# Optimization experiments

Hardware: AMD Instinct MI355X
Metric: run time of the kernel (lower is better)

## Reference

```python
import jax, jax.numpy as jnp
import numpy as np

N, E, G = 20000, 320000, 256      # nodes, edges, graphs per batch
IN, D, P = 128, 256, 16           # input_dim, out_dim, n_prot
EPS, R, TEMP = 1e-7, 0.5, 0.2


def setup_inputs() -> dict:
    key = jax.random.key(0)
    ks = jax.random.split(key, 9)
    x = jax.random.normal(ks[0], (N, IN), jnp.float32)
    edge_index = jax.random.randint(ks[1], (2, E), 0, N)
    batch = jnp.sort(jax.random.randint(ks[2], (N,), 0, G))
    def w(k, sh):
        fan_in = sh[0]
        return jax.random.normal(k, sh, jnp.float32) * (1.0 / fan_in) ** 0.5
    return {
        "x": x, "edge_index": edge_index, "batch": batch,
        "W1": w(ks[3], (IN, D)), "b1": jnp.zeros((D,), jnp.float32),
        "W2": w(ks[4], (D, D)), "b2": jnp.zeros((D,), jnp.float32),
        "Wm1": w(ks[5], (2 * D, D)), "bm1": jnp.zeros((D,), jnp.float32),
        "Wm2": w(ks[6], (D, 1)), "bm2": jnp.zeros((1,), jnp.float32),
        "prototypes": jax.random.normal(ks[7], (P, D), jnp.float32),
    }


def _cosine(a, b):
    # prototype_distances: cosine similarity with zero-norm -> eps fixup (eval path, no softmax)
    na = jnp.linalg.norm(a, axis=1)
    na = jnp.where(na == 0, na + EPS, na)
    nb = jnp.linalg.norm(b, axis=1)
    nb = jnp.where(nb == 0, nb + EPS, nb)
    return jnp.einsum('ik,jk->ij', a, b) / (na[:, None] * nb[None, :])


def _encoder(x, src, dst, batch, W1, b1, W2, b2, atten=None):
    # 2-layer GIN: h' = relu((h + sum_{j->i} atten_ji * h_j) W + b); graph emb = sum pool
    def conv(h, W, b):
        msg = h[src]                                   # [E, d]
        if atten is not None:
            msg = msg * atten                          # [E, 1] broadcast
        agg = h + jax.ops.segment_sum(msg, dst, num_segments=N)
        return jax.nn.relu(agg @ W + b)
    h = conv(x, W1, b1)
    h = conv(h, W2, b2)
    g = jax.ops.segment_sum(h, batch, num_segments=G)  # [G, D]
    return g, h


def reference(x, edge_index, batch, W1, b1, W2, b2, Wm1, bm1, Wm2, bm2, prototypes):
    src, dst = edge_index[0], edge_index[1]
    graph_embs, node_embs = _encoder(x, src, dst, batch, W1, b1, W2, b2)

    # eval path: assign each graph to nearest prototype by cosine similarity
    sim0 = _cosine(graph_embs, prototypes)             # [G, P]
    assign_prot = jnp.argmax(sim0, axis=1)             # [G]

    # sample_subgraph (eval: plain sigmoid, no gumbel noise)
    node_proto = prototypes[assign_prot[batch]]        # [N, D]
    h = jnp.concatenate([node_embs, node_proto], axis=-1)
    node_prob = jax.nn.relu(h @ Wm1 + bm1) @ Wm2 + bm2  # [N, 1]
    node_bern = jax.nn.sigmoid(node_prob)              # [N, 1]
    edge_bern = node_bern[src] * node_bern[dst]        # [E, 1]

    x2 = x * node_bern
    subgraph_embs, _ = _encoder(x2, src, dst, batch, W1, b1, W2, b2, atten=edge_bern)

    similarity = _cosine(subgraph_embs, prototypes)    # [G, P]

    # NCE loss
    a2 = jnp.argmax(similarity, axis=1)
    onehot = jax.nn.one_hot(a2, P, dtype=similarity.dtype)
    se = jnp.exp(similarity / TEMP)
    pos = (se * onehot).sum(axis=1)
    neg = (se * (1.0 - onehot)).sum(axis=1)
    NCE_loss = -jnp.log(pos / neg).mean()

    # KL regularizers
    nb = node_bern
    KL_node = (nb * jnp.log(nb / R + EPS)
               + (1 - nb) * jnp.log((1 - nb) / (1 - R + EPS) + EPS)).mean()
    eb = edge_bern
    KL_edge = (eb * jnp.log(eb / (R * R) + EPS)
               + (1 - eb) * jnp.log((1 - eb) / (1 - R * R + EPS) + EPS)).mean()
    KL_loss = KL_node + KL_edge

    data_sim = _cosine(subgraph_embs, subgraph_embs)   # [G, G]
    return (KL_loss, NCE_loss, similarity, node_bern, edge_bern,
            data_sim, subgraph_embs, node_embs)
```

## Files before the change

kernel.cpp:

```cpp
#include <hip/hip_runtime.h>
#include <cmath>
#include <cstdint>

#define DINL __device__ __forceinline__

namespace {

constexpr int Nn = 20000, Ee = 320000, Gg = 256, Dd = 256, Pp = 16;
constexpr int Npad = 20096;
constexpr float EPSf = 1e-7f, Rf = 0.5f, TEMPf = 0.2f;

typedef unsigned short u16;
typedef __attribute__((ext_vector_type(8))) short short8;
typedef __attribute__((ext_vector_type(4))) float floatx4;

DINL float waveSum(float x) {
#pragma unroll
  for (int off = 32; off > 0; off >>= 1) x += __shfl_xor(x, off, 64);
  return x;
}

DINL u16 f2bf(float f) {
  unsigned u = __float_as_uint(f);
  unsigned r = u + 0x7fffu + ((u >> 16) & 1u);
  return (u16)(r >> 16);
}
DINL float bf2f(u16 h) { return __uint_as_float(((unsigned)h) << 16); }

__global__ void k_deg(const int* __restrict__ dst, int* __restrict__ deg) {
  int e = blockIdx.x * 256 + threadIdx.x;
  if (e < Ee) atomicAdd(&deg[dst[e]], 1);
}

__global__ __launch_bounds__(1024) void k_scan(const int* __restrict__ deg,
                                               int* __restrict__ offs) {
  __shared__ int part[1024];
  int tid = threadIdx.x;
  const int chunk = (Nn + 1023) >> 10;
  int start = tid * chunk;
  int s = 0;
  for (int k = 0; k < chunk; k++) { int i = start + k; if (i < Nn) s += deg[i]; }
  part[tid] = s;
  __syncthreads();
  for (int off = 1; off < 1024; off <<= 1) {
    int v = (tid >= off) ? part[tid - off] : 0;
    __syncthreads();
    part[tid] += v;
    __syncthreads();
  }
  int run = (tid == 0) ? 0 : part[tid - 1];
  for (int k = 0; k < chunk; k++) {
    int i = start + k;
    if (i < Nn) { offs[i] = run; run += deg[i]; }
  }
  if (start < Nn && start + chunk >= Nn) offs[Nn] = run;
}

__global__ void k_fill(const int* __restrict__ src, const int* __restrict__ dst,
                       const int* __restrict__ offs, int* __restrict__ cursor,
                       int* __restrict__ csr) {
  int e = blockIdx.x * 256 + threadIdx.x;
  if (e < Ee) {
    int d = dst[e];
    int pos = atomicAdd(&cursor[d], 1);
    csr[offs[d] + pos] = src[e];
  }
}

__global__ void k_goff(const int* __restrict__ batch, int* __restrict__ goff) {
  int i = blockIdx.x * 256 + threadIdx.x;
  if (i >= Nn) return;
  int bi = batch[i];
  int bp = (i == 0) ? -1 : batch[i - 1];
  for (int g = bp + 1; g <= bi; ++g) goff[g] = i;
  if (i == Nn - 1)
    for (int g = bi + 1; g <= Gg; ++g) goff[g] = Nn;
}

template <int DIM, int EPL, bool INBF>
DINL void slice(float r[EPL], const void* __restrict__ hv, int row, int ce) {
  if constexpr (INBF) {
    const u16* p = (const u16*)hv + (size_t)row * DIM + ce;
    ushort4 u = *(const ushort4*)p;
    r[0] = bf2f(u.x); r[1] = bf2f(u.y); r[2] = bf2f(u.z); r[3] = bf2f(u.w);
  } else {
    const float* p = (const float*)hv + (size_t)row * DIM + ce;
    float2 u = *(const float2*)p;
    r[0] = u.x; r[1] = u.y;
  }
}

template <int DIM, int MODE, bool INBF, bool OSPL>
__global__ __launch_bounds__(256) void k_aggc(
    const void* __restrict__ hv, const float* __restrict__ nb,
    const int* __restrict__ offs, const int* __restrict__ csr,
    u16* __restrict__ oh, u16* __restrict__ ol) {
  constexpr int EPL = INBF ? 4 : 2;
  constexpr int COLS = EPL * 16;
  constexpr int CHUNKS = DIM / COLS;
  int c = (int)(blockIdx.x % CHUNKS);
  int grp = (int)(blockIdx.x / CHUNKS);
  int wv = threadIdx.x >> 6, lane = threadIdx.x & 63;
  int sub = lane >> 4, l = lane & 15;
  int node = grp * 16 + wv * 4 + sub;
  if (node >= Nn) return;
  int ce = c * COLS + l * EPL;
  float self[EPL], ts[EPL];
  slice<DIM, EPL, INBF>(self, hv, node, ce);
#pragma unroll
  for (int j = 0; j < EPL; j++) ts[j] = 0.f;
  int beg = offs[node], end = offs[node + 1];
  int k = beg;
  for (; k + 4 <= end; k += 4) {
    int s0 = csr[k], s1 = csr[k + 1], s2 = csr[k + 2], s3 = csr[k + 3];
    float r0[EPL], r1[EPL], r2[EPL], r3[EPL];
    slice<DIM, EPL, INBF>(r0, hv, s0, ce);
    slice<DIM, EPL, INBF>(r1, hv, s1, ce);
    slice<DIM, EPL, INBF>(r2, hv, s2, ce);
    slice<DIM, EPL, INBF>(r3, hv, s3, ce);
    if (MODE == 0) {
#pragma unroll
      for (int j = 0; j < EPL; j++) ts[j] += (r0[j] + r1[j]) + (r2[j] + r3[j]);
    } else {
      float w0 = nb[s0], w1 = nb[s1], w2 = nb[s2], w3 = nb[s3];
      if (MODE == 1) { w0 *= w0; w1 *= w1; w2 *= w2; w3 *= w3; }
#pragma unroll
      for (int j = 0; j < EPL; j++)
        ts[j] += (w0 * r0[j] + w1 * r1[j]) + (w2 * r2[j] + w3 * r3[j]);
    }
  }
  for (; k < end; k++) {
    int s = csr[k];
    float r[EPL];
    slice<DIM, EPL, INBF>(r, hv, s, ce);
    if (MODE == 0) {
#pragma unroll
      for (int j = 0; j < EPL; j++) ts[j] += r[j];
    } else {
      float wq = nb[s];
      if (MODE == 1) wq *= wq;
#pragma unroll
      for (int j = 0; j < EPL; j++) ts[j] += wq * r[j];
    }
  }
  float val[EPL];
  if (MODE == 0) {
#pragma unroll
    for (int j = 0; j < EPL; j++) val[j] = self[j] + ts[j];
  } else if (MODE == 1) {
    float wi = nb[node];
#pragma unroll
    for (int j = 0; j < EPL; j++) val[j] = wi * (self[j] + ts[j]);
  } else {
    float wi = nb[node];
#pragma unroll
    for (int j = 0; j < EPL; j++) val[j] = self[j] + wi * ts[j];
  }
  u16 hs[EPL], ls[EPL];
#pragma unroll
  for (int j = 0; j < EPL; j++) {
    hs[j] = f2bf(val[j]);
    if (OSPL) ls[j] = f2bf(val[j] - bf2f(hs[j]));
  }
  u16* po = oh + (size_t)node * DIM + ce;
  if constexpr (EPL == 2) {
    *(ushort2*)po = make_ushort2(hs[0], hs[1]);
  } else {
    *(ushort4*)po = make_ushort4(hs[0], hs[1], hs[2], hs[3]);
  }
  if constexpr (OSPL) {
    u16* pl = ol + (size_t)node * DIM + ce;
    if constexpr (EPL == 2) {
      *(ushort2*)pl = make_ushort2(ls[0], ls[1]);
    } else {
      *(ushort4*)pl = make_ushort4(ls[0], ls[1], ls[2], ls[3]);
    }
  }
}

template <int K, bool SPLIT, int MODE>
__global__ __launch_bounds__(256) void k_mm(
    const u16* __restrict__ Ah, const u16* __restrict__ Al,
    const u16* __restrict__ Bh, const u16* __restrict__ Bl,
    const float* __restrict__ bias,
    float* __restrict__ outF, u16* __restrict__ outH, u16* __restrict__ outL,
    const float* __restrict__ pc, const int* __restrict__ batch,
    const int* __restrict__ assign, const float* __restrict__ Wm2,
    float* __restrict__ prob) {
  constexpr int SK = 40;
  __shared__ u16 AsH[128 * SK];
  __shared__ u16 AsL[SPLIT ? 128 * SK : 16];
  __shared__ u16 BsH[64 * SK];
  __shared__ u16 BsL[SPLIT ? 64 * SK : 16];
  __shared__ int ap_s[128];
  int t = threadIdx.x;
  int rowBase = blockIdx.y * 128, colBase = blockIdx.x * 64;
  if (MODE == 1 && t < 128) {
    int r = rowBase + t;
    ap_s[t] = (r < Nn) ? assign[batch[r]] : 0;
  }
  int lane = t & 63, wv = t >> 6;
  int quad = lane >> 4, l16 = lane & 15;
  int wm = wv * 32;
  floatx4 acc[2][4];
#pragma unroll
  for (int mt = 0; mt < 2; mt++)
#pragma unroll
    for (int nt = 0; nt < 4; nt++) acc[mt][nt] = (floatx4){0.f, 0.f, 0.f, 0.f};

  int ar = t >> 1;
  int akh = (t & 1) * 16;
  const u16* agH = Ah + (size_t)(rowBase + ar) * K + akh;
  const u16* agL = Al + (size_t)(rowBase + ar) * K + akh;
  int bn = t >> 2;
  int bko = (t & 3) * 8;
  const u16* bgH = Bh + (size_t)(colBase + bn) * K + bko;
  const u16* bgL = Bl + (size_t)(colBase + bn) * K + bko;

  for (int k0 = 0; k0 < K; k0 += 32) {
    uint4 a0 = *(const uint4*)(agH + k0);
    uint4 a1 = *(const uint4*)(agH + k0 + 8);
    uint4 b0 = *(const uint4*)(bgH + k0);
    uint4 a0l, a1l, b0l;
    if constexpr (SPLIT) {
      a0l = *(const uint4*)(agL + k0);
      a1l = *(const uint4*)(agL + k0 + 8);
      b0l = *(const uint4*)(bgL + k0);
    }
    __syncthreads();
    *(uint4*)&AsH[ar * SK + akh] = a0;
    *(uint4*)&AsH[ar * SK + akh + 8] = a1;
    *(uint4*)&BsH[bn * SK + bko] = b0;
    if constexpr (SPLIT) {
      *(uint4*)&AsL[ar * SK + akh] = a0l;
      *(uint4*)&AsL[ar * SK + akh + 8] = a1l;
      *(uint4*)&BsL[bn * SK + bko] = b0l;
    }
    __syncthreads();
    short8 aH[2], aL[2], bH[4], bL[4];
#pragma unroll
    for (int mt = 0; mt < 2; mt++) {
      int off = (wm + mt * 16 + l16) * SK + quad * 8;
      aH[mt] = *(const short8*)&AsH[off];
      if (SPLIT) aL[mt] = *(const short8*)&AsL[off];
    }
#pragma unroll
    for (int nt = 0; nt < 4; nt++) {
      int off = (nt * 16 + l16) * SK + quad * 8;
      bH[nt] = *(const short8*)&BsH[off];
      if (SPLIT) bL[nt] = *(const short8*)&BsL[off];
    }
#pragma unroll
    for (int mt = 0; mt < 2; mt++)
#pragma unroll
      for (int nt = 0; nt < 4; nt++) {
        acc[mt][nt] = __builtin_amdgcn_mfma_f32_16x16x32_bf16(aH[mt], bH[nt], acc[mt][nt], 0, 0, 0);
        if constexpr (SPLIT) {
          acc[mt][nt] = __builtin_amdgcn_mfma_f32_16x16x32_bf16(aH[mt], bL[nt], acc[mt][nt], 0, 0, 0);
          acc[mt][nt] = __builtin_amdgcn_mfma_f32_16x16x32_bf16(aL[mt], bH[nt], acc[mt][nt], 0, 0, 0);
        }
      }
  }

  if constexpr (MODE == 0) {
#pragma unroll
    for (int mt = 0; mt < 2; mt++)
#pragma unroll
      for (int nt = 0; nt < 4; nt++) {
        int col = colBase + nt * 16 + l16;
        float bv = bias[col];
#pragma unroll
        for (int r = 0; r < 4; r++) {
          int row = rowBase + wm + mt * 16 + quad * 4 + r;
          if (row < Nn) {
            float v = fmaxf(acc[mt][nt][r] + bv, 0.f);
            size_t o = (size_t)row * 256 + col;
            if (outF) outF[o] = v;
            if (outH) {
              u16 hh = f2bf(v);
              outH[o] = hh;
              if (outL) outL[o] = f2bf(v - bf2f(hh));
            }
          }
        }
      }
  } else {
#pragma unroll
    for (int mt = 0; mt < 2; mt++) {
      float part[4] = {0.f, 0.f, 0.f, 0.f};
#pragma unroll
      for (int nt = 0; nt < 4; nt++) {
        int col = colBase + nt * 16 + l16;
        float wmv = Wm2[col];
#pragma unroll
        for (int r = 0; r < 4; r++) {
          int lr = wm + mt * 16 + quad * 4 + r;
          int ap = ap_s[lr];
          float tv = fmaxf(acc[mt][nt][r] + pc[ap * 256 + col], 0.f);
          part[r] += tv * wmv;
        }
      }
#pragma unroll
      for (int r = 0; r < 4; r++) {
#pragma unroll
        for (int off = 1; off < 16; off <<= 1) part[r] += __shfl_xor(part[r], off, 64);
        if (l16 == 0) {
          int row = rowBase + wm + mt * 16 + quad * 4 + r;
          if (row < Nn) atomicAdd(&prob[row], part[r]);
        }
      }
    }
  }
}

__global__ __launch_bounds__(64) void k_pool(const float* __restrict__ h,
                                             const int* __restrict__ goff,
                                             float* __restrict__ gout,
                                             float* __restrict__ gout2) {
  int g = blockIdx.x, q = blockIdx.y, c = q * 64 + threadIdx.x;
  int beg = goff[g], end = goff[g + 1];
  float s = 0.f;
  for (int n = beg; n < end; ++n) s += h[(size_t)n * Dd + c];
  gout[g * Dd + c] = s;
  if (gout2 != nullptr) gout2[g * Dd + c] = s;
}

__global__ __launch_bounds__(64) void k_pc(const float* __restrict__ proto,
                                           const float* __restrict__ Wm1,
                                           const float* __restrict__ bm1,
                                           float* __restrict__ pc,
                                           float* __restrict__ pnorm) {
  int p = blockIdx.x, q = blockIdx.y, t = threadIdx.x;
  int cc = q * 64 + t;
  float s = bm1[cc];
  for (int k = 0; k < Dd; k++) s += proto[p * Dd + k] * Wm1[(size_t)(Dd + k) * Dd + cc];
  pc[p * Dd + cc] = s;
  if (q == 0) {
    float4 v = ((const float4*)(proto + (size_t)p * Dd))[t];
    float nsq = waveSum(v.x * v.x + v.y * v.y + v.z * v.z + v.w * v.w);
    if (t == 0) {
      float n = sqrtf(nsq);
      pnorm[p] = (n == 0.f) ? EPSf : n;
    }
  }
}

__global__ __launch_bounds__(64) void k_assign(const float* __restrict__ ge,
                                               const float* __restrict__ proto,
                                               const float* __restrict__ pnorm,
                                               int* __restrict__ assign) {
  int g = blockIdx.x, lane = threadIdx.x;
  float4 v = *(const float4*)(ge + (size_t)g * Dd + lane * 4);
  float na = sqrtf(waveSum(v.x * v.x + v.y * v.y + v.z * v.z + v.w * v.w));
  if (na == 0.f) na = EPSf;
  float best = -1e30f;
  int bi = 0;
#pragma unroll
  for (int p = 0; p < Pp; p++) {
    float4 w = *(const float4*)(proto + (size_t)p * Dd + lane * 4);
    float d = waveSum(v.x * w.x + v.y * w.y + v.z * w.z + v.w * w.w);
    float sim = d / (na * pnorm[p]);
    if (sim > best) { best = sim; bi = p; }
  }
  if (lane == 0) assign[g] = bi;
}

__global__ __launch_bounds__(64) void k_simnce(const float* __restrict__ se,
                                               const float* __restrict__ proto,
                                               const float* __restrict__ pnorm,
                                               float* __restrict__ osim,
                                               float* __restrict__ snorm,
                                               float* __restrict__ nceAcc) {
  int g = blockIdx.x, lane = threadIdx.x;
  float4 v = *(const float4*)(se + (size_t)g * Dd + lane * 4);
  float na = sqrtf(waveSum(v.x * v.x + v.y * v.y + v.z * v.z + v.w * v.w));
  if (na == 0.f) na = EPSf;
  float sims[Pp];
#pragma unroll
  for (int p = 0; p < Pp; p++) {
    float4 w = *(const float4*)(proto + (size_t)p * Dd + lane * 4);
    float d = waveSum(v.x * w.x + v.y * w.y + v.z * w.z + v.w * w.w);
    float sim = d / (na * pnorm[p]);
    sims[p] = sim;
    if (lane == p) osim[g * Pp + p] = sim;
  }
  float best = sims[0];
  int bi = 0;
#pragma unroll
  for (int p = 1; p < Pp; p++) {
    if (sims[p] > best) { best = sims[p]; bi = p; }
  }
  float pos = 0.f, neg = 0.f;
#pragma unroll
  for (int p = 0; p < Pp; p++) {
    float e = expf(sims[p] / TEMPf);
    if (p == bi) pos = e; else neg += e;
  }
  float lg = -logf(pos / neg);
  if (lane == 0) {
    atomicAdd(nceAcc, lg);
    snorm[g] = na;
  }
}

__global__ void k_bern(const float* __restrict__ prob, const float* __restrict__ bm2,
                       float* __restrict__ ob, float* __restrict__ accs) {
  int i = blockIdx.x * 256 + threadIdx.x;
  float val = 0.f;
  if (i < Nn) {
    float z = prob[i] + bm2[0];
    float p = 1.f / (1.f + expf(-z));
    ob[i] = p;
    const float invA = 1.f / Rf, invB = 1.f / (1.f - Rf + EPSf);
    val = p * logf(p * invA + EPSf) + (1.f - p) * logf((1.f - p) * invB + EPSf);
  }
  val = waveSum(val);
  __shared__ float wsum[4];
  int lane = threadIdx.x & 63, wvv = threadIdx.x >> 6;
  if (lane == 0) wsum[wvv] = val;
  __syncthreads();
  if (threadIdx.x == 0) atomicAdd(accs, wsum[0] + wsum[1] + wsum[2] + wsum[3]);
}

__global__ void k_eb(const int* __restrict__ src, const int* __restrict__ dst,
                     const float* __restrict__ nb, float* __restrict__ oe,
                     float* __restrict__ accs) {
  int e = blockIdx.x * 256 + threadIdx.x;
  float val = 0.f;
  if (e < Ee) {
    float v = nb[src[e]] * nb[dst[e]];
    oe[e] = v;
    const float invA = 1.f / (Rf * Rf), invB = 1.f / (1.f - Rf * Rf + EPSf);
    val = v * logf(v * invA + EPSf) + (1.f - v) * logf((1.f - v) * invB + EPSf);
  }
  val = waveSum(val);
  __shared__ float wsum[4];
  int lane = threadIdx.x & 63, wvv = threadIdx.x >> 6;
  if (lane == 0) wsum[wvv] = val;
  __syncthreads();
  if (threadIdx.x == 0) atomicAdd(accs + 1, wsum[0] + wsum[1] + wsum[2] + wsum[3]);
}

__global__ void k_fin(const float* __restrict__ accs, float* __restrict__ o_kl,
                      float* __restrict__ o_nce) {
  o_kl[0] = accs[0] / (float)Nn + accs[1] / (float)Ee;
  o_nce[0] = accs[2] / (float)Gg;
}

__global__ void k_datasim(const float* __restrict__ S, const float* __restrict__ snorm,
                          float* __restrict__ out) {
  __shared__ float si[Dd];
  int i = blockIdx.x, j = threadIdx.x;
  si[j] = S[(size_t)i * Dd + j];
  __syncthreads();
  const float4* rj = (const float4*)(S + (size_t)j * Dd);
  const float4* sif = (const float4*)si;
  float d = 0.f;
#pragma unroll 4
  for (int k = 0; k < Dd / 4; k++) {
    float4 a = sif[k];
    float4 b = rj[k];
    d += a.x * b.x + a.y * b.y + a.z * b.z + a.w * b.w;
  }
  out[(size_t)i * Gg + j] = d / (snorm[i] * snorm[j]);
}

__global__ void k_splitw(const float* __restrict__ W, u16* __restrict__ th,
                         u16* __restrict__ tl, int K) {
  int idx = blockIdx.x * 256 + threadIdx.x;
  if (idx >= K * 256) return;
  int k = idx >> 8, n = idx & 255;
  float v = W[idx];
  u16 h = f2bf(v);
  th[(size_t)n * K + k] = h;
  tl[(size_t)n * K + k] = f2bf(v - bf2f(h));
}

__global__ void k_cvtbf4(const float4* __restrict__ x, ushort4* __restrict__ o, int n4) {
  int i = blockIdx.x * 256 + threadIdx.x;
  if (i < n4) {
    float4 v = x[i];
    o[i] = make_ushort4(f2bf(v.x), f2bf(v.y), f2bf(v.z), f2bf(v.w));
  }
}

}

extern "C" void kernel_launch(void* const* d_in, const int* in_sizes, int n_in,
                              void* d_out, int out_size, void* d_ws, size_t ws_size,
                              hipStream_t stream) {
  const float* x = (const float*)d_in[0];
  const int* ei = (const int*)d_in[1];
  const int* batch = (const int*)d_in[2];
  const float* W1 = (const float*)d_in[3];
  const float* b1 = (const float*)d_in[4];
  const float* W2 = (const float*)d_in[5];
  const float* b2 = (const float*)d_in[6];
  const float* Wm1 = (const float*)d_in[7];
  const float* bm1 = (const float*)d_in[8];
  const float* Wm2 = (const float*)d_in[9];
  const float* bm2 = (const float*)d_in[10];
  const float* proto = (const float*)d_in[11];
  const int* src = ei;
  const int* dst = ei + Ee;

  float* out = (float*)d_out;
  float* o_kl = out;
  float* o_nce = out + 1;
  float* o_sim = out + 2;
  float* o_nb = o_sim + Gg * Pp;
  float* o_eb = o_nb + Nn;
  float* o_ds = o_eb + Ee;
  float* o_sg = o_ds + Gg * Gg;
  float* o_ne = o_sg + Gg * Dd;

  char* w = (char*)d_ws;
  auto take = [&](size_t bytes) -> char* {
    char* p = w;
    w += (bytes + 255) & ~(size_t)255;
    return p;
  };
  const size_t halfR = (size_t)Npad * 256 * 2;
  float* bufB = (float*)take((size_t)Npad * 256 * 4);
  char* R2 = take(2 * halfR);
  u16* A1h = (u16*)R2;
  u16* A1l = (u16*)(R2 + (size_t)Npad * 128 * 2);
  u16* A2h = (u16*)R2;
  u16* A2l = (u16*)(R2 + halfR);
  u16* h1b = (u16*)R2;
  u16* a2bh = (u16*)(R2 + halfR);
  char* R3 = take(2 * halfR);
  u16* neh = (u16*)R3;
  u16* nel = (u16*)(R3 + halfR);
  u16* a1bh = (u16*)R3;
  u16* xbf = (u16*)(R3 + halfR);

  int* csr = (int*)take((size_t)Ee * 4);
  int* deg = (int*)take((size_t)Nn * 4);
  int* cursor = (int*)take((size_t)Nn * 4);
  int* offs = (int*)take((size_t)(Nn + 1) * 4);
  int* goff = (int*)take((size_t)(Gg + 1) * 4);
  float* gemb = (float*)take((size_t)Gg * Dd * 4);
  float* sgemb = (float*)take((size_t)Gg * Dd * 4);
  float* pcb = (float*)take((size_t)Pp * Dd * 4);
  float* pnorm = (float*)take(Pp * 4);
  int* assign = (int*)take(Gg * 4);
  float* snorm = (float*)take(Gg * 4);
  float* prob = (float*)take(Nn * 4);
  float* accs = (float*)take(16);
  u16* W1th = (u16*)take((size_t)256 * 128 * 2);
  u16* W1tl = (u16*)take((size_t)256 * 128 * 2);
  u16* W2th = (u16*)take((size_t)256 * 256 * 2);
  u16* W2tl = (u16*)take((size_t)256 * 256 * 2);
  u16* Wm1th = (u16*)take((size_t)256 * 256 * 2);
  u16* Wm1tl = (u16*)take((size_t)256 * 256 * 2);

  hipMemsetAsync(deg, 0, 2 * 80128, stream);
  hipMemsetAsync(prob, 0, 80128 + 16, stream);

  const int eB = (Ee + 255) / 256;
  const int nB = (Nn + 255) / 256;
  dim3 gmm(4, 157);

  k_deg<<<eB, 256, 0, stream>>>(dst, deg);
  k_scan<<<1, 1024, 0, stream>>>(deg, offs);
  k_fill<<<eB, 256, 0, stream>>>(src, dst, offs, cursor, csr);
  k_goff<<<nB, 256, 0, stream>>>(batch, goff);
  k_pc<<<dim3(Pp, 4), 64, 0, stream>>>(proto, Wm1, bm1, pcb, pnorm);
  k_splitw<<<(128 * 256 + 255) / 256, 256, 0, stream>>>(W1, W1th, W1tl, 128);
  k_splitw<<<(256 * 256 + 255) / 256, 256, 0, stream>>>(W2, W2th, W2tl, 256);
  k_splitw<<<(256 * 256 + 255) / 256, 256, 0, stream>>>(Wm1, Wm1th, Wm1tl, 256);

  k_aggc<128, 0, false, true><<<1250 * 4, 256, 0, stream>>>(x, nullptr, offs, csr, A1h, A1l);
  k_mm<128, true, 0><<<gmm, 256, 0, stream>>>(A1h, A1l, W1th, W1tl, b1, bufB, nullptr,
                                              nullptr, nullptr, nullptr, nullptr,
                                              nullptr, nullptr);
  k_aggc<256, 0, false, true><<<1250 * 8, 256, 0, stream>>>(bufB, nullptr, offs, csr, A2h, A2l);
  k_mm<256, true, 0><<<gmm, 256, 0, stream>>>(A2h, A2l, W2th, W2tl, b2, o_ne, neh, nel,
                                              nullptr, nullptr, nullptr, nullptr,
                                              nullptr);
  k_pool<<<dim3(Gg, 4), 64, 0, stream>>>(o_ne, goff, gemb, nullptr);
  k_assign<<<Gg, 64, 0, stream>>>(gemb, proto, pnorm, assign);
  k_mm<256, true, 1><<<gmm, 256, 0, stream>>>(neh, nel, Wm1th, Wm1tl, nullptr, nullptr,
                                              nullptr, nullptr, pcb, batch, assign,
                                              Wm2, prob);
  k_bern<<<nB, 256, 0, stream>>>(prob, bm2, o_nb, accs);
  k_eb<<<eB, 256, 0, stream>>>(src, dst, o_nb, o_eb, accs);

  k_cvtbf4<<<(Nn * 128 / 4 + 255) / 256, 256, 0, stream>>>((const float4*)x,
                                                           (ushort4*)xbf, Nn * 128 / 4);
  k_aggc<128, 1, true, false><<<1250 * 2, 256, 0, stream>>>(xbf, o_nb, offs, csr, a1bh, nullptr);
  k_mm<128, false, 0><<<gmm, 256, 0, stream>>>(a1bh, nullptr, W1th, nullptr, b1, nullptr,
                                               h1b, nullptr, nullptr, nullptr, nullptr,
                                               nullptr, nullptr);
  k_aggc<256, 2, true, false><<<1250 * 4, 256, 0, stream>>>(h1b, o_nb, offs, csr, a2bh, nullptr);
  k_mm<256, false, 0><<<gmm, 256, 0, stream>>>(a2bh, nullptr, W2th, nullptr, b2, bufB,
                                               nullptr, nullptr, nullptr, nullptr,
                                               nullptr, nullptr, nullptr);
  k_pool<<<dim3(Gg, 4), 64, 0, stream>>>(bufB, goff, sgemb, o_sg);

  k_simnce<<<Gg, 64, 0, stream>>>(sgemb, proto, pnorm, o_sim, snorm, accs + 2);
  k_fin<<<1, 1, 0, stream>>>(accs, o_kl, o_nce);
  k_datasim<<<Gg, 256, 0, stream>>>(sgemb, snorm, o_ds);
}
```

Measured before the change: 473.3 us.

## Fuse small kernels and add nontemporal loads/stores across aggregation and GEMM

```diff
diff --git a/kernel.cpp b/kernel.cpp
--- a/kernel.cpp
+++ b/kernel.cpp
@@ -13,6 +13,8 @@
 typedef unsigned short u16;
 typedef __attribute__((ext_vector_type(8))) short short8;
 typedef __attribute__((ext_vector_type(4))) float floatx4;
+typedef __attribute__((ext_vector_type(2))) unsigned int u2v;
+typedef __attribute__((ext_vector_type(4))) unsigned int u4v;
 
 DINL float waveSum(float x) {
 #pragma unroll
@@ -32,28 +34,40 @@
   if (e < Ee) atomicAdd(&deg[dst[e]], 1);
 }
 
-__global__ __launch_bounds__(1024) void k_scan(const int* __restrict__ deg,
-                                               int* __restrict__ offs) {
-  __shared__ int part[1024];
+__global__ __launch_bounds__(1024) void k_pre(const int* __restrict__ deg,
+                                              int* __restrict__ offs,
+                                              const int* __restrict__ batch,
+                                              int* __restrict__ goff) {
   int tid = threadIdx.x;
-  const int chunk = (Nn + 1023) >> 10;
-  int start = tid * chunk;
-  int s = 0;
-  for (int k = 0; k < chunk; k++) { int i = start + k; if (i < Nn) s += deg[i]; }
-  part[tid] = s;
-  __syncthreads();
-  for (int off = 1; off < 1024; off <<= 1) {
-    int v = (tid >= off) ? part[tid - off] : 0;
+  if (blockIdx.x == 0) {
+    __shared__ int part[1024];
+    const int chunk = (Nn + 1023) >> 10;
+    int start = tid * chunk;
+    int s = 0;
+    for (int k = 0; k < chunk; k++) { int i = start + k; if (i < Nn) s += deg[i]; }
+    part[tid] = s;
     __syncthreads();
-    part[tid] += v;
-    __syncthreads();
-  }
-  int run = (tid == 0) ? 0 : part[tid - 1];
-  for (int k = 0; k < chunk; k++) {
-    int i = start + k;
-    if (i < Nn) { offs[i] = run; run += deg[i]; }
-  }
-  if (start < Nn && start + chunk >= Nn) offs[Nn] = run;
+    for (int off = 1; off < 1024; off <<= 1) {
+      int v = (tid >= off) ? part[tid - off] : 0;
+      __syncthreads();
+      part[tid] += v;
+      __syncthreads();
+    }
+    int run = (tid == 0) ? 0 : part[tid - 1];
+    for (int k = 0; k < chunk; k++) {
+      int i = start + k;
+      if (i < Nn) { offs[i] = run; run += deg[i]; }
+    }
+    if (start < Nn && start + chunk >= Nn) offs[Nn] = run;
+  } else {
+    for (int i = tid; i < Nn; i += 1024) {
+      int bi = batch[i];
+      int bp = (i == 0) ? -1 : batch[i - 1];
+      for (int g = bp + 1; g <= bi; ++g) goff[g] = i;
+      if (i == Nn - 1)
+        for (int g = bi + 1; g <= Gg; ++g) goff[g] = Nn;
+    }
+  }
 }
 
 __global__ void k_fill(const int* __restrict__ src, const int* __restrict__ dst,
@@ -65,16 +79,6 @@
     int pos = atomicAdd(&cursor[d], 1);
     csr[offs[d] + pos] = src[e];
   }
-}
-
-__global__ void k_goff(const int* __restrict__ batch, int* __restrict__ goff) {
-  int i = blockIdx.x * 256 + threadIdx.x;
-  if (i >= Nn) return;
-  int bi = batch[i];
-  int bp = (i == 0) ? -1 : batch[i - 1];
-  for (int g = bp + 1; g <= bi; ++g) goff[g] = i;
-  if (i == Nn - 1)
-    for (int g = bi + 1; g <= Gg; ++g) goff[g] = Nn;
 }
 
 template <int DIM, int EPL, bool INBF>
@@ -164,21 +168,29 @@
   }
   u16* po = oh + (size_t)node * DIM + ce;
   if constexpr (EPL == 2) {
-    *(ushort2*)po = make_ushort2(hs[0], hs[1]);
+    unsigned v = (unsigned)hs[0] | ((unsigned)hs[1] << 16);
+    __builtin_nontemporal_store(v, (unsigned*)po);
   } else {
-    *(ushort4*)po = make_ushort4(hs[0], hs[1], hs[2], hs[3]);
+    u2v v;
+    v.x = (unsigned)hs[0] | ((unsigned)hs[1] << 16);
+    v.y = (unsigned)hs[2] | ((unsigned)hs[3] << 16);
+    __builtin_nontemporal_store(v, (u2v*)po);
   }
   if constexpr (OSPL) {
     u16* pl = ol + (size_t)node * DIM + ce;
     if constexpr (EPL == 2) {
-      *(ushort2*)pl = make_ushort2(ls[0], ls[1]);
+      unsigned v = (unsigned)ls[0] | ((unsigned)ls[1] << 16);
+      __builtin_nontemporal_store(v, (unsigned*)pl);
     } else {
-      *(ushort4*)pl = make_ushort4(ls[0], ls[1], ls[2], ls[3]);
-    }
-  }
-}
-
-template <int K, bool SPLIT, int MODE>
+      u2v v;
+      v.x = (unsigned)ls[0] | ((unsigned)ls[1] << 16);
+      v.y = (unsigned)ls[2] | ((unsigned)ls[3] << 16);
+      __builtin_nontemporal_store(v, (u2v*)pl);
+    }
+  }
+}
+
+template <int K, bool SPLIT, int MODE, bool NTO>
 __global__ __launch_bounds__(256) void k_mm(
     const u16* __restrict__ Ah, const u16* __restrict__ Al,
     const u16* __restrict__ Bh, const u16* __restrict__ Bl,
@@ -218,23 +230,23 @@
   const u16* bgL = Bl + (size_t)(colBase + bn) * K + bko;
 
   for (int k0 = 0; k0 < K; k0 += 32) {
-    uint4 a0 = *(const uint4*)(agH + k0);
-    uint4 a1 = *(const uint4*)(agH + k0 + 8);
-    uint4 b0 = *(const uint4*)(bgH + k0);
-    uint4 a0l, a1l, b0l;
+    u4v a0 = __builtin_nontemporal_load((const u4v*)(agH + k0));
+    u4v a1 = __builtin_nontemporal_load((const u4v*)(agH + k0 + 8));
+    u4v b0 = *(const u4v*)(bgH + k0);
+    u4v a0l, a1l, b0l;
     if constexpr (SPLIT) {
-      a0l = *(const uint4*)(agL + k0);
-      a1l = *(const uint4*)(agL + k0 + 8);
-      b0l = *(const uint4*)(bgL + k0);
+      a0l = __builtin_nontemporal_load((const u4v*)(agL + k0));
+      a1l = __builtin_nontemporal_load((const u4v*)(agL + k0 + 8));
+      b0l = *(const u4v*)(bgL + k0);
     }
     __syncthreads();
-    *(uint4*)&AsH[ar * SK + akh] = a0;
-    *(uint4*)&AsH[ar * SK + akh + 8] = a1;
-    *(uint4*)&BsH[bn * SK + bko] = b0;
+    *(u4v*)&AsH[ar * SK + akh] = a0;
+    *(u4v*)&AsH[ar * SK + akh + 8] = a1;
+    *(u4v*)&BsH[bn * SK + bko] = b0;
     if constexpr (SPLIT) {
-      *(uint4*)&AsL[ar * SK + akh] = a0l;
-      *(uint4*)&AsL[ar * SK + akh + 8] = a1l;
-      *(uint4*)&BsL[bn * SK + bko] = b0l;
+      *(u4v*)&AsL[ar * SK + akh] = a0l;
+      *(u4v*)&AsL[ar * SK + akh + 8] = a1l;
+      *(u4v*)&BsL[bn * SK + bko] = b0l;
     }
     __syncthreads();
     short8 aH[2], aL[2], bH[4], bL[4];
@@ -275,11 +287,19 @@
           if (row < Nn) {
             float v = fmaxf(acc[mt][nt][r] + bv, 0.f);
             size_t o = (size_t)row * 256 + col;
-            if (outF) outF[o] = v;
+            if (outF) {
+              if (NTO) __builtin_nontemporal_store(v, &outF[o]);
+              else outF[o] = v;
+            }
             if (outH) {
               u16 hh = f2bf(v);
-              outH[o] = hh;
-              if (outL) outL[o] = f2bf(v - bf2f(hh));
+              if (NTO) __builtin_nontemporal_store(hh, &outH[o]);
+              else outH[o] = hh;
+              if (outL) {
+                u16 ll = f2bf(v - bf2f(hh));
+                if (NTO) __builtin_nontemporal_store(ll, &outL[o]);
+                else outL[o] = ll;
+              }
             }
           }
         }
@@ -313,16 +333,81 @@
   }
 }
 
-__global__ __launch_bounds__(64) void k_pool(const float* __restrict__ h,
-                                             const int* __restrict__ goff,
-                                             float* __restrict__ gout,
-                                             float* __restrict__ gout2) {
-  int g = blockIdx.x, q = blockIdx.y, c = q * 64 + threadIdx.x;
+__global__ __launch_bounds__(256) void k_poolassign(
+    const float* __restrict__ h, const int* __restrict__ goff,
+    const float* __restrict__ proto, const float* __restrict__ pnorm,
+    int* __restrict__ assign) {
+  __shared__ float row[Dd];
+  int g = blockIdx.x, c = threadIdx.x;
   int beg = goff[g], end = goff[g + 1];
   float s = 0.f;
-  for (int n = beg; n < end; ++n) s += h[(size_t)n * Dd + c];
-  gout[g * Dd + c] = s;
-  if (gout2 != nullptr) gout2[g * Dd + c] = s;
+  for (int n = beg; n < end; ++n)
+    s += __builtin_nontemporal_load(&h[(size_t)n * Dd + c]);
+  row[c] = s;
+  __syncthreads();
+  if (c < 64) {
+    float4 v = ((const float4*)row)[c];
+    float na = sqrtf(waveSum(v.x * v.x + v.y * v.y + v.z * v.z + v.w * v.w));
+    if (na == 0.f) na = EPSf;
+    float best = -1e30f;
+    int bi = 0;
+#pragma unroll
+    for (int p = 0; p < Pp; p++) {
+      float4 w = *(const float4*)(proto + (size_t)p * Dd + c * 4);
+      float d = waveSum(v.x * w.x + v.y * w.y + v.z * w.z + v.w * w.w);
+      float sim = d / (na * pnorm[p]);
+      if (sim > best) { best = sim; bi = p; }
+    }
+    if (c == 0) assign[g] = bi;
+  }
+}
+
+__global__ __launch_bounds__(256) void k_poolsim(
+    const float* __restrict__ h, const int* __restrict__ goff,
+    const float* __restrict__ proto, const float* __restrict__ pnorm,
+    float* __restrict__ o_sg, float* __restrict__ sgemb,
+    float* __restrict__ osim, float* __restrict__ snorm,
+    float* __restrict__ nceAcc) {
+  __shared__ float row[Dd];
+  int g = blockIdx.x, c = threadIdx.x;
+  int beg = goff[g], end = goff[g + 1];
+  float s = 0.f;
+  for (int n = beg; n < end; ++n)
+    s += __builtin_nontemporal_load(&h[(size_t)n * Dd + c]);
+  row[c] = s;
+  o_sg[(size_t)g * Dd + c] = s;
+  sgemb[(size_t)g * Dd + c] = s;
+  __syncthreads();
+  if (c < 64) {
+    float4 v = ((const float4*)row)[c];
+    float na = sqrtf(waveSum(v.x * v.x + v.y * v.y + v.z * v.z + v.w * v.w));
+    if (na == 0.f) na = EPSf;
+    float sims[Pp];
+#pragma unroll
+    for (int p = 0; p < Pp; p++) {
+      float4 w = *(const float4*)(proto + (size_t)p * Dd + c * 4);
+      float d = waveSum(v.x * w.x + v.y * w.y + v.z * w.z + v.w * w.w);
+      float sim = d / (na * pnorm[p]);
+      sims[p] = sim;
+      if (c == p) osim[g * Pp + p] = sim;
+    }
+    float best = sims[0];
+    int bi = 0;
+#pragma unroll
+    for (int p = 1; p < Pp; p++) {
+      if (sims[p] > best) { best = sims[p]; bi = p; }
+    }
+    float pos = 0.f, neg = 0.f;
+#pragma unroll
+    for (int p = 0; p < Pp; p++) {
+      float e = expf(sims[p] / TEMPf);
+      if (p == bi) pos = e; else neg += e;
+    }
+    if (c == 0) {
+      atomicAdd(nceAcc, -logf(pos / neg));
+      snorm[g] = na;
+    }
+  }
 }
 
 __global__ __launch_bounds__(64) void k_pc(const float* __restrict__ proto,
@@ -345,100 +430,58 @@
   }
 }
 
-__global__ __launch_bounds__(64) void k_assign(const float* __restrict__ ge,
-                                               const float* __restrict__ proto,
-                                               const float* __restrict__ pnorm,
-                                               int* __restrict__ assign) {
-  int g = blockIdx.x, lane = threadIdx.x;
-  float4 v = *(const float4*)(ge + (size_t)g * Dd + lane * 4);
-  float na = sqrtf(waveSum(v.x * v.x + v.y * v.y + v.z * v.z + v.w * v.w));
-  if (na == 0.f) na = EPSf;
-  float best = -1e30f;
-  int bi = 0;
-#pragma unroll
-  for (int p = 0; p < Pp; p++) {
-    float4 w = *(const float4*)(proto + (size_t)p * Dd + lane * 4);
-    float d = waveSum(v.x * w.x + v.y * w.y + v.z * w.z + v.w * w.w);
-    float sim = d / (na * pnorm[p]);
-    if (sim > best) { best = sim; bi = p; }
-  }
-  if (lane == 0) assign[g] = bi;
-}
-
-__global__ __launch_bounds__(64) void k_simnce(const float* __restrict__ se,
-                                               const float* __restrict__ proto,
-                                               const float* __restrict__ pnorm,
-                                               float* __restrict__ osim,
-                                               float* __restrict__ snorm,
-                                               float* __restrict__ nceAcc) {
-  int g = blockIdx.x, lane = threadIdx.x;
-  float4 v = *(const float4*)(se + (size_t)g * Dd + lane * 4);
-  float na = sqrtf(waveSum(v.x * v.x + v.y * v.y + v.z * v.z + v.w * v.w));
-  if (na == 0.f) na = EPSf;
-  float sims[Pp];
-#pragma unroll
-  for (int p = 0; p < Pp; p++) {
-    float4 w = *(const float4*)(proto + (size_t)p * Dd + lane * 4);
-    float d = waveSum(v.x * w.x + v.y * w.y + v.z * w.z + v.w * w.w);
-    float sim = d / (na * pnorm[p]);
-    sims[p] = sim;
-    if (lane == p) osim[g * Pp + p] = sim;
-  }
-  float best = sims[0];
-  int bi = 0;
-#pragma unroll
-  for (int p = 1; p < Pp; p++) {
-    if (sims[p] > best) { best = sims[p]; bi = p; }
-  }
-  float pos = 0.f, neg = 0.f;
-#pragma unroll
-  for (int p = 0; p < Pp; p++) {
-    float e = expf(sims[p] / TEMPf);
-    if (p == bi) pos = e; else neg += e;
-  }
-  float lg = -logf(pos / neg);
-  if (lane == 0) {
-    atomicAdd(nceAcc, lg);
-    snorm[g] = na;
-  }
-}
-
-__global__ void k_bern(const float* __restrict__ prob, const float* __restrict__ bm2,
-                       float* __restrict__ ob, float* __restrict__ accs) {
-  int i = blockIdx.x * 256 + threadIdx.x;
-  float val = 0.f;
-  if (i < Nn) {
-    float z = prob[i] + bm2[0];
-    float p = 1.f / (1.f + expf(-z));
-    ob[i] = p;
-    const float invA = 1.f / Rf, invB = 1.f / (1.f - Rf + EPSf);
-    val = p * logf(p * invA + EPSf) + (1.f - p) * logf((1.f - p) * invB + EPSf);
-  }
-  val = waveSum(val);
-  __shared__ float wsum[4];
-  int lane = threadIdx.x & 63, wvv = threadIdx.x >> 6;
-  if (lane == 0) wsum[wvv] = val;
-  __syncthreads();
-  if (threadIdx.x == 0) atomicAdd(accs, wsum[0] + wsum[1] + wsum[2] + wsum[3]);
-}
-
-__global__ void k_eb(const int* __restrict__ src, const int* __restrict__ dst,
-                     const float* __restrict__ nb, float* __restrict__ oe,
-                     float* __restrict__ accs) {
-  int e = blockIdx.x * 256 + threadIdx.x;
-  float val = 0.f;
-  if (e < Ee) {
-    float v = nb[src[e]] * nb[dst[e]];
-    oe[e] = v;
-    const float invA = 1.f / (Rf * Rf), invB = 1.f / (1.f - Rf * Rf + EPSf);
-    val = v * logf(v * invA + EPSf) + (1.f - v) * logf((1.f - v) * invB + EPSf);
-  }
-  val = waveSum(val);
-  __shared__ float wsum[4];
-  int lane = threadIdx.x & 63, wvv = threadIdx.x >> 6;
-  if (lane == 0) wsum[wvv] = val;
-  __syncthreads();
-  if (threadIdx.x == 0) atomicAdd(accs + 1, wsum[0] + wsum[1] + wsum[2] + wsum[3]);
+__global__ void k_berneb(const float* __restrict__ prob, const float* __restrict__ bm2,
+                         const int* __restrict__ src, const int* __restrict__ dst,
+                         const float* __restrict__ x, u16* __restrict__ xbf,
+                         float* __restrict__ ob, float* __restrict__ oe,
+                         float* __restrict__ accs) {
+  const int nB = (Nn + 255) / 256, eB = (Ee + 255) / 256;
+  int b = blockIdx.x;
+  if (b < nB) {
+    int i = b * 256 + threadIdx.x;
+    float val = 0.f;
+    if (i < Nn) {
+      float z = prob[i] + bm2[0];
+      float p = 1.f / (1.f + expf(-z));
+      ob[i] = p;
+      const float invA = 1.f / Rf, invB = 1.f / (1.f - Rf + EPSf);
+      val = p * logf(p * invA + EPSf) + (1.f - p) * logf((1.f - p) * invB + EPSf);
+    }
+    val = waveSum(val);
+    __shared__ float wsum[4];
+    int lane = threadIdx.x & 63, wvv = threadIdx.x >> 6;
+    if (lane == 0) wsum[wvv] = val;
+    __syncthreads();
+    if (threadIdx.x == 0) atomicAdd(accs, wsum[0] + wsum[1] + wsum[2] + wsum[3]);
+  } else if (b < nB + eB) {
+    int e = (b - nB) * 256 + threadIdx.x;
+    float val = 0.f;
+    if (e < Ee) {
+      float zs = prob[src[e]] + bm2[0];
+      float zd = prob[dst[e]] + bm2[0];
+      float ps = 1.f / (1.f + expf(-zs));
+      float pd = 1.f / (1.f + expf(-zd));
+      float v = ps * pd;
+      __builtin_nontemporal_store(v, &oe[e]);
+      const float invA = 1.f / (Rf * Rf), invB = 1.f / (1.f - Rf * Rf + EPSf);
+      val = v * logf(v * invA + EPSf) + (1.f - v) * logf((1.f - v) * invB + EPSf);
+    }
+    val = waveSum(val);
+    __shared__ float wsum2[4];
+    int lane = threadIdx.x & 63, wvv = threadIdx.x >> 6;
+    if (lane == 0) wsum2[wvv] = val;
+    __syncthreads();
+    if (threadIdx.x == 0) atomicAdd(accs + 1, wsum2[0] + wsum2[1] + wsum2[2] + wsum2[3]);
+  } else {
+    int i = (b - nB - eB) * 256 + threadIdx.x;
+    if (i < Nn * 128 / 4) {
+      float4 v = ((const float4*)x)[i];
+      u2v o;
+      o.x = (unsigned)f2bf(v.x) | ((unsigned)f2bf(v.y) << 16);
+      o.y = (unsigned)f2bf(v.z) | ((unsigned)f2bf(v.w) << 16);
+      __builtin_nontemporal_store(o, (u2v*)&xbf[(size_t)i * 4]);
+    }
+  }
 }
 
 __global__ void k_fin(const float* __restrict__ accs, float* __restrict__ o_kl,
@@ -465,23 +508,30 @@
   out[(size_t)i * Gg + j] = d / (snorm[i] * snorm[j]);
 }
 
-__global__ void k_splitw(const float* __restrict__ W, u16* __restrict__ th,
-                         u16* __restrict__ tl, int K) {
+__global__ void k_prep(const float* __restrict__ W1, const float* __restrict__ W2,
+                       const float* __restrict__ Wm1, u16* __restrict__ W1th,
+                       u16* __restrict__ W1tl, u16* __restrict__ W2th,
+                       u16* __restrict__ W2tl, u16* __restrict__ Wm1th,
+                       u16* __restrict__ Wm1tl) {
   int idx = blockIdx.x * 256 + threadIdx.x;
-  if (idx >= K * 256) return;
+  const float* W;
+  u16 *th, *tl;
+  int K;
+  if (idx < 128 * 256) {
+    W = W1; th = W1th; tl = W1tl; K = 128;
+  } else if (idx < 128 * 256 + 256 * 256) {
+    idx -= 128 * 256;
+    W = W2; th = W2th; tl = W2tl; K = 256;
+  } else {
+    idx -= 128 * 256 + 256 * 256;
+    if (idx >= 256 * 256) return;
+    W = Wm1; th = Wm1th; tl = Wm1tl; K = 256;
+  }
   int k = idx >> 8, n = idx & 255;
   float v = W[idx];
   u16 h = f2bf(v);
   th[(size_t)n * K + k] = h;
   tl[(size_t)n * K + k] = f2bf(v - bf2f(h));
-}
-
-__global__ void k_cvtbf4(const float4* __restrict__ x, ushort4* __restrict__ o, int n4) {
-  int i = blockIdx.x * 256 + threadIdx.x;
-  if (i < n4) {
-    float4 v = x[i];
-    o[i] = make_ushort4(f2bf(v.x), f2bf(v.y), f2bf(v.z), f2bf(v.w));
-  }
 }
 
 }
@@ -540,7 +590,6 @@
   int* cursor = (int*)take((size_t)Nn * 4);
   int* offs = (int*)take((size_t)(Nn + 1) * 4);
   int* goff = (int*)take((size_t)(Gg + 1) * 4);
-  float* gemb = (float*)take((size_t)Gg * Dd * 4);
   float* sgemb = (float*)take((size_t)Gg * Dd * 4);
   float* pcb = (float*)take((size_t)Pp * Dd * 4);
   float* pnorm = (float*)take(Pp * 4);
@@ -563,43 +612,36 @@
   dim3 gmm(4, 157);
 
   k_deg<<<eB, 256, 0, stream>>>(dst, deg);
-  k_scan<<<1, 1024, 0, stream>>>(deg, offs);
+  k_pre<<<2, 1024, 0, stream>>>(deg, offs, batch, goff);
   k_fill<<<eB, 256, 0, stream>>>(src, dst, offs, cursor, csr);
-  k_goff<<<nB, 256, 0, stream>>>(batch, goff);
   k_pc<<<dim3(Pp, 4), 64, 0, stream>>>(proto, Wm1, bm1, pcb, pnorm);
-  k_splitw<<<(128 * 256 + 255) / 256, 256, 0, stream>>>(W1, W1th, W1tl, 128);
-  k_splitw<<<(256 * 256 + 255) / 256, 256, 0, stream>>>(W2, W2th, W2tl, 256);
-  k_splitw<<<(256 * 256 + 255) / 256, 256, 0, stream>>>(Wm1, Wm1th, Wm1tl, 256);
+  k_prep<<<640, 256, 0, stream>>>(W1, W2, Wm1, W1th, W1tl, W2th, W2tl, Wm1th, Wm1tl);
 
   k_aggc<128, 0, false, true><<<1250 * 4, 256, 0, stream>>>(x, nullptr, offs, csr, A1h, A1l);
-  k_mm<128, true, 0><<<gmm, 256, 0, stream>>>(A1h, A1l, W1th, W1tl, b1, bufB, nullptr,
-                                              nullptr, nullptr, nullptr, nullptr,
-                                              nullptr, nullptr);
+  k_mm<128, true, 0, false><<<gmm, 256, 0, stream>>>(A1h, A1l, W1th, W1tl, b1, bufB,
+                                                     nullptr, nullptr, nullptr, nullptr,
+                                                     nullptr, nullptr, nullptr);
   k_aggc<256, 0, false, true><<<1250 * 8, 256, 0, stream>>>(bufB, nullptr, offs, csr, A2h, A2l);
-  k_mm<256, true, 0><<<gmm, 256, 0, stream>>>(A2h, A2l, W2th, W2tl, b2, o_ne, neh, nel,
-                                              nullptr, nullptr, nullptr, nullptr,
-                                              nullptr);
-  k_pool<<<dim3(Gg, 4), 64, 0, stream>>>(o_ne, goff, gemb, nullptr);
-  k_assign<<<Gg, 64, 0, stream>>>(gemb, proto, pnorm, assign);
-  k_mm<256, true, 1><<<gmm, 256, 0, stream>>>(neh, nel, Wm1th, Wm1tl, nullptr, nullptr,
-                                              nullptr, nullptr, pcb, batch, assign,
-                                              Wm2, prob);
-  k_bern<<<nB, 256, 0, stream>>>(prob, bm2, o_nb, accs);
-  k_eb<<<eB, 256, 0, stream>>>(src, dst, o_nb, o_eb, accs);
-
-  k_cvtbf4<<<(Nn * 128 / 4 + 255) / 256, 256, 0, stream>>>((const float4*)x,
-                                                           (ushort4*)xbf, Nn * 128 / 4);
+  k_mm<256, true, 0, true><<<gmm, 256, 0, stream>>>(A2h, A2l, W2th, W2tl, b2, o_ne, neh,
+                                                    nel, nullptr, nullptr, nullptr,
+                                                    nullptr, nullptr);
+  k_poolassign<<<Gg, 256, 0, stream>>>(o_ne, goff, proto, pnorm, assign);
+  k_mm<256, true, 1, false><<<gmm, 256, 0, stream>>>(neh, nel, Wm1th, Wm1tl, nullptr,
+                                                     nullptr, nullptr, nullptr, pcb,
+                                                     batch, assign, Wm2, prob);
+  k_berneb<<<nB + eB + (Nn * 128 / 4 + 255) / 256, 256, 0, stream>>>(
+      prob, bm2, src, dst, x, xbf, o_nb, o_eb, accs);
+
   k_aggc<128, 1, true, false><<<1250 * 2, 256, 0, stream>>>(xbf, o_nb, offs, csr, a1bh, nullptr);
-  k_mm<128, false, 0><<<gmm, 256, 0, stream>>>(a1bh, nullptr, W1th, nullptr, b1, nullptr,
-                                               h1b, nullptr, nullptr, nullptr, nullptr,
-                                               nullptr, nullptr);
+  k_mm<128, false, 0, false><<<gmm, 256, 0, stream>>>(a1bh, nullptr, W1th, nullptr, b1,
+                                                      nullptr, h1b, nullptr, nullptr,
+                                                      nullptr, nullptr, nullptr, nullptr);
   k_aggc<256, 2, true, false><<<1250 * 4, 256, 0, stream>>>(h1b, o_nb, offs, csr, a2bh, nullptr);
-  k_mm<256, false, 0><<<gmm, 256, 0, stream>>>(a2bh, nullptr, W2th, nullptr, b2, bufB,
-                                               nullptr, nullptr, nullptr, nullptr,
-                                               nullptr, nullptr, nullptr);
-  k_pool<<<dim3(Gg, 4), 64, 0, stream>>>(bufB, goff, sgemb, o_sg);
-
-  k_simnce<<<Gg, 64, 0, stream>>>(sgemb, proto, pnorm, o_sim, snorm, accs + 2);
+  k_mm<256, false, 0, true><<<gmm, 256, 0, stream>>>(a2bh, nullptr, W2th, nullptr, b2,
+                                                     bufB, nullptr, nullptr, nullptr,
+                                                     nullptr, nullptr, nullptr, nullptr);
+  k_poolsim<<<Gg, 256, 0, stream>>>(bufB, goff, proto, pnorm, o_sg, sgemb, o_sim, snorm,
+                                    accs + 2);
   k_fin<<<1, 1, 0, stream>>>(accs, o_kl, o_nce);
   k_datasim<<<Gg, 256, 0, stream>>>(sgemb, snorm, o_ds);
 }
```

Result: slower. 584.3 us (+23.5%).
